# Kernel optimization log

Hardware: AMD Instinct MI355X
Metric: run time of the kernel (lower is better)

## Reference

```python
import jax, jax.numpy as jnp
import numpy as np

BATCH, FLAT_IN, PROJ_DIM, HEADS, ACT_DIM = 2048, 512, 256, 16384, 64


def setup_inputs() -> dict:
    key = jax.random.key(0)
    k1, k2, k3, k4 = jax.random.split(key, 4)
    state = jax.random.normal(k1, (BATCH, FLAT_IN), dtype=jnp.float32)
    random_projection = jax.random.normal(k2, (FLAT_IN, PROJ_DIM), dtype=jnp.float32)
    memories = jax.random.normal(k3, (HEADS, PROJ_DIM), dtype=jnp.float32)
    logits = jax.random.normal(k4, (HEADS, ACT_DIM), dtype=jnp.float32)
    return {"state": state, "random_projection": random_projection,
            "memories": memories, "logits": logits}


def reference(state, random_projection, memories, logits):
    # state: [B, flat_in] -> projected [B, proj_dim] (proj_dim branch of __call__)
    s = state.reshape(state.shape[0], -1) @ random_projection
    # sum(state[:,None] * memories[None,:], -1) == dot-product similarity GEMM
    similarities = jnp.einsum('bd,hd->bh', s, memories)  # [B, heads]
    closest = jnp.argmax(similarities, axis=1)           # [B]
    return logits[closest]                                # [B, act_dim]
```

## Files before the change

kernel.cpp:

```cpp
#include <hip/hip_runtime.h>

#define BATCH    2048
#define FLAT_IN  512
#define PROJ_DIM 256
#define HEADS    16384
#define ACT_DIM  64

typedef __attribute__((ext_vector_type(8))) short short8;
typedef _Float16 half8 __attribute__((ext_vector_type(8)));
typedef __attribute__((ext_vector_type(4))) float floatx4;

__device__ __forceinline__ unsigned short f2bf(float x) {
  unsigned u = __float_as_uint(x);
  u += 0x7fff + ((u >> 16) & 1);
  return (unsigned short)(u >> 16);
}
__device__ __forceinline__ float bf2f(unsigned short b) {
  return __uint_as_float(((unsigned)b) << 16);
}
__device__ __forceinline__ unsigned short f2h(float x) {
  _Float16 h = (_Float16)x;
  return __builtin_bit_cast(unsigned short, h);
}

__device__ __forceinline__ unsigned pack_key(float v, int h) {
  unsigned u = __float_as_uint(v);
  unsigned m = (unsigned)(((int)u) >> 31) | 0x80000000u;
  return ((u ^ m) & 0xFFFFC000u) | (unsigned)(16383 - h);
}

#define GLDS16(g, l)                                                          \
  __builtin_amdgcn_global_load_lds(                                           \
      (__attribute__((address_space(1))) void*)(void*)(g),                    \
      (__attribute__((address_space(3))) void*)(l), 16, 0, 0)

__global__ __launch_bounds__(256) void prep(
    const float* __restrict__ state, const float* __restrict__ rp,
    unsigned short* __restrict__ st_hi, unsigned short* __restrict__ st_mid,
    unsigned short* __restrict__ rpT_hi, unsigned short* __restrict__ rpT_mid)
{
  const int tid = threadIdx.x;
  const int b = blockIdx.x;
  if (b < 1024) {
    int i = b * 256 + tid;
    float4 v = ((const float4*)state)[i];
    ushort4 h, m;
    h.x = f2bf(v.x); m.x = f2bf(v.x - bf2f(h.x));
    h.y = f2bf(v.y); m.y = f2bf(v.y - bf2f(h.y));
    h.z = f2bf(v.z); m.z = f2bf(v.z - bf2f(h.z));
    h.w = f2bf(v.w); m.w = f2bf(v.w - bf2f(h.w));
    ((ushort4*)st_hi)[i]  = h;
    ((ushort4*)st_mid)[i] = m;
  } else {
    __shared__ float t[64][65];
    int bid = b - 1024;
    int k0 = (bid >> 2) * 64, n0 = (bid & 3) * 64;
#pragma unroll
    for (int it = 0; it < 16; ++it) {
      int lin = it * 256 + tid;
      int kr = lin >> 6, nc = lin & 63;
      t[kr][nc] = rp[(size_t)(k0 + kr) * PROJ_DIM + n0 + nc];
    }
    __syncthreads();
#pragma unroll
    for (int it = 0; it < 16; ++it) {
      int lin = it * 256 + tid;
      int nr = lin >> 6, kc = lin & 63;
      float v = t[kc][nr];
      unsigned short hh = f2bf(v);
      rpT_hi [(size_t)(n0 + nr) * FLAT_IN + k0 + kc] = hh;
      rpT_mid[(size_t)(n0 + nr) * FLAT_IN + k0 + kc] = f2bf(v - bf2f(hh));
    }
  }
}

__global__ __launch_bounds__(256, 2) void gemm_conv(
    const unsigned short* __restrict__ Ahi, const unsigned short* __restrict__ Amid,
    const unsigned short* __restrict__ Bhi, const unsigned short* __restrict__ Bmid,
    const float* __restrict__ mem,
    float* __restrict__ S, unsigned short* __restrict__ Sf16,
    unsigned short* __restrict__ mem_f16)
{
  const int tid = threadIdx.x;
  if (blockIdx.x >= 128) {
    int i2 = (blockIdx.x - 128) * 256 + tid;
    float4 x = ((const float4*)mem)[2 * i2];
    float4 y = ((const float4*)mem)[2 * i2 + 1];
    short8 o;
    o[0] = (short)f2h(x.x); o[1] = (short)f2h(x.y);
    o[2] = (short)f2h(x.z); o[3] = (short)f2h(x.w);
    o[4] = (short)f2h(y.x); o[5] = (short)f2h(y.y);
    o[6] = (short)f2h(y.z); o[7] = (short)f2h(y.w);
    ((short8*)mem_f16)[i2] = o;
    return;
  }

  __shared__ __align__(16) unsigned short sm[4][64 * 64];
  const int lane = tid & 63, w = tid >> 6;
  const int quad = lane >> 4, col = lane & 15;
  const int wm = (w >> 1) * 32, wn = (w & 1) * 32;
  const int g = blockIdx.x;
  const int m0 = (g & 31) * 64, n0 = (g >> 5) * 64;

  floatx4 acc[2][2];
#pragma unroll
  for (int i = 0; i < 2; ++i)
#pragma unroll
    for (int j = 0; j < 2; ++j) {
      acc[i][j][0] = 0.f; acc[i][j][1] = 0.f;
      acc[i][j][2] = 0.f; acc[i][j][3] = 0.f;
    }

  const int P0 = tid, P1 = tid + 256;
  const int r0 = P0 >> 3, kl0 = (P0 & 7) ^ (r0 & 7);
  const int r1 = P1 >> 3, kl1 = (P1 & 7) ^ (r1 & 7);

  for (int kc = 0; kc < FLAT_IN; kc += 64) {
    GLDS16(Ahi  + (size_t)(m0 + r0) * FLAT_IN + kc + kl0 * 8, &sm[0][P0 * 8]);
    GLDS16(Ahi  + (size_t)(m0 + r1) * FLAT_IN + kc + kl1 * 8, &sm[0][P1 * 8]);
    GLDS16(Amid + (size_t)(m0 + r0) * FLAT_IN + kc + kl0 * 8, &sm[1][P0 * 8]);
    GLDS16(Amid + (size_t)(m0 + r1) * FLAT_IN + kc + kl1 * 8, &sm[1][P1 * 8]);
    GLDS16(Bhi  + (size_t)(n0 + r0) * FLAT_IN + kc + kl0 * 8, &sm[2][P0 * 8]);
    GLDS16(Bhi  + (size_t)(n0 + r1) * FLAT_IN + kc + kl1 * 8, &sm[2][P1 * 8]);
    GLDS16(Bmid + (size_t)(n0 + r0) * FLAT_IN + kc + kl0 * 8, &sm[3][P0 * 8]);
    GLDS16(Bmid + (size_t)(n0 + r1) * FLAT_IN + kc + kl1 * 8, &sm[3][P1 * 8]);
    __syncthreads();

#pragma unroll
    for (int ks = 0; ks < 2; ++ks) {
      short8 bf[2][2];
#pragma unroll
      for (int j = 0; j < 2; ++j) {
        int rr = wn + j * 16 + col;
        int off = rr * 64 + (((ks * 4 + quad) ^ (rr & 7)) * 8);
        bf[j][0] = *(const short8*)&sm[2][off];
        bf[j][1] = *(const short8*)&sm[3][off];
      }
#pragma unroll
      for (int i = 0; i < 2; ++i) {
        int rr = wm + i * 16 + col;
        int off = rr * 64 + (((ks * 4 + quad) ^ (rr & 7)) * 8);
        short8 a0 = *(const short8*)&sm[0][off];
        short8 a1 = *(const short8*)&sm[1][off];
#pragma unroll
        for (int j = 0; j < 2; ++j) {
          acc[i][j] = __builtin_amdgcn_mfma_f32_16x16x32_bf16(a0, bf[j][0], acc[i][j], 0, 0, 0);
          acc[i][j] = __builtin_amdgcn_mfma_f32_16x16x32_bf16(a0, bf[j][1], acc[i][j], 0, 0, 0);
          acc[i][j] = __builtin_amdgcn_mfma_f32_16x16x32_bf16(a1, bf[j][0], acc[i][j], 0, 0, 0);
        }
      }
    }
    __syncthreads();
  }

#pragma unroll
  for (int i = 0; i < 2; ++i)
#pragma unroll
    for (int j = 0; j < 2; ++j)
#pragma unroll
      for (int r = 0; r < 4; ++r) {
        int row = m0 + wm + i * 16 + quad * 4 + r;
        int c   = n0 + wn + j * 16 + col;
        float v = acc[i][j][r];
        S   [(size_t)row * PROJ_DIM + c] = v;
        Sf16[(size_t)row * PROJ_DIM + c] = f2h(v);
      }
}

__global__ __launch_bounds__(512, 2) void sim_topk(
    const unsigned short* __restrict__ Af16,
    const unsigned short* __restrict__ Bf16,
    unsigned* __restrict__ part1)
{
  __shared__ __align__(16) unsigned short smA[256 * 64];
  __shared__ __align__(16) unsigned short smB[256 * 64];
  const int tid = threadIdx.x;
  const int lane = tid & 63, w = tid >> 6;
  const int quad = lane >> 4, col = lane & 15;
  const int wm = (w >> 2) * 128, wn = (w & 3) * 64;
  const int hc = blockIdx.x;
  const int h0 = hc * 256;
  const int m0 = blockIdx.y * 256;

  floatx4 acc[8][4];
#pragma unroll
  for (int i = 0; i < 8; ++i)
#pragma unroll
    for (int j = 0; j < 4; ++j) {
      acc[i][j][0] = 0.f; acc[i][j][1] = 0.f;
      acc[i][j][2] = 0.f; acc[i][j][3] = 0.f;
    }

  int rs[4], kl[4];
#pragma unroll
  for (int t = 0; t < 4; ++t) {
    int P = t * 512 + tid;
    rs[t] = P >> 3; kl[t] = (P & 7) ^ (rs[t] & 7);
  }

  for (int kc = 0; kc < PROJ_DIM; kc += 64) {
#pragma unroll
    for (int t = 0; t < 4; ++t)
      GLDS16(Af16 + (size_t)(m0 + rs[t]) * PROJ_DIM + kc + kl[t] * 8,
             &smA[(t * 512 + tid) * 8]);
#pragma unroll
    for (int t = 0; t < 4; ++t)
      GLDS16(Bf16 + (size_t)(h0 + rs[t]) * PROJ_DIM + kc + kl[t] * 8,
             &smB[(t * 512 + tid) * 8]);
    __syncthreads();

#pragma unroll
    for (int ks = 0; ks < 2; ++ks) {
      half8 a[8], bfr[4];
#pragma unroll
      for (int j = 0; j < 4; ++j) {
        int rr = wn + j * 16 + col;
        int off = rr * 64 + (((ks * 4 + quad) ^ (rr & 7)) * 8);
        bfr[j] = *(const half8*)&smB[off];
      }
#pragma unroll
      for (int i = 0; i < 8; ++i) {
        int rr = wm + i * 16 + col;
        int off = rr * 64 + (((ks * 4 + quad) ^ (rr & 7)) * 8);
        a[i] = *(const half8*)&smA[off];
      }
#pragma unroll
      for (int i = 0; i < 8; ++i)
#pragma unroll
        for (int j = 0; j < 4; ++j)
          acc[i][j] = __builtin_amdgcn_mfma_f32_16x16x32_f16(a[i], bfr[j], acc[i][j], 0, 0, 0);
    }
    __syncthreads();
  }

#pragma unroll
  for (int i = 0; i < 8; ++i)
#pragma unroll
    for (int r = 0; r < 4; ++r) {
      unsigned best = pack_key(acc[i][0][r], h0 + wn + col);
#pragma unroll
      for (int j = 1; j < 4; ++j) {
        unsigned k = pack_key(acc[i][j][r], h0 + wn + j * 16 + col);
        best = best > k ? best : k;
      }
#pragma unroll
      for (int m = 1; m <= 8; m <<= 1) {
        unsigned o = (unsigned)__shfl_xor((int)best, m);
        best = best > o ? best : o;
      }
      if (col == 0) {
        int row = m0 + wm + i * 16 + quad * 4 + r;
        part1[((size_t)row * 64 + hc) * 4 + (w & 3)] = best;
      }
    }
}

__global__ __launch_bounds__(64) void finalize(
    const unsigned* __restrict__ part1, const float* __restrict__ S,
    const float* __restrict__ Mem, const float* __restrict__ logits,
    float* __restrict__ out)
{
  const int row  = blockIdx.x;
  const int lane = threadIdx.x;

  unsigned k[4];
#pragma unroll
  for (int t = 0; t < 4; ++t)
    k[t] = part1[(size_t)row * 256 + t * 64 + lane];

  int cand[4]; float4 mv[4];
#pragma unroll
  for (int t = 0; t < 4; ++t) {
    unsigned lv = k[0];
#pragma unroll
    for (int q = 1; q < 4; ++q) lv = lv > k[q] ? lv : k[q];
#pragma unroll
    for (int d = 32; d; d >>= 1) {
      unsigned o = (unsigned)__shfl_xor((int)lv, d);
      lv = lv > o ? lv : o;
    }
    cand[t] = 16383 - (int)(lv & 16383u);
    mv[t] = ((const float4*)(Mem + (size_t)cand[t] * PROJ_DIM))[lane];
#pragma unroll
    for (int q = 0; q < 4; ++q)
      if (k[q] == lv) k[q] = 0;
  }

  float4 sv = ((const float4*)(S + (size_t)row * PROJ_DIM))[lane];
  float bestv = -3.4e38f; int besth = 0x7fffffff;
#pragma unroll
  for (int t = 0; t < 4; ++t) {
    float d = sv.x * mv[t].x + sv.y * mv[t].y + sv.z * mv[t].z + sv.w * mv[t].w;
#pragma unroll
    for (int s = 32; s; s >>= 1) d += __shfl_xor(d, s);
    if (d > bestv || (d == bestv && cand[t] < besth)) { bestv = d; besth = cand[t]; }
  }
  out[(size_t)row * ACT_DIM + lane] = logits[(size_t)besth * ACT_DIM + lane];
}

extern "C" void kernel_launch(void* const* d_in, const int* in_sizes, int n_in,
                              void* d_out, int out_size, void* d_ws, size_t ws_size,
                              hipStream_t stream) {
  const float* state  = (const float*)d_in[0];
  const float* rp     = (const float*)d_in[1];
  const float* mem    = (const float*)d_in[2];
  const float* logits = (const float*)d_in[3];
  float* out = (float*)d_out;

  char* ws = (char*)d_ws;
  unsigned short* st_hi   = (unsigned short*)(ws);
  unsigned short* st_mid  = (unsigned short*)(ws + (2u  << 20));
  unsigned short* rpT_hi  = (unsigned short*)(ws + (4u  << 20));
  unsigned short* rpT_mid = (unsigned short*)(ws + (4u  << 20) + (256u << 10));
  unsigned short* mem_f16 = (unsigned short*)(ws + (8u  << 20));
  float*          s       = (float*)(ws + (16u << 20));
  unsigned short* s_f16   = (unsigned short*)(ws + (18u << 20));
  unsigned*       part1   = (unsigned*)(ws + (20u << 20));

  prep<<<1056, 256, 0, stream>>>(state, rp, st_hi, st_mid, rpT_hi, rpT_mid);

  gemm_conv<<<2176, 256, 0, stream>>>(st_hi, st_mid, rpT_hi, rpT_mid, mem,
                                      s, s_f16, mem_f16);

  sim_topk<<<dim3(64, 8), 512, 0, stream>>>(s_f16, mem_f16, part1);

  finalize<<<BATCH, 64, 0, stream>>>(part1, s, mem, logits, out);
}
```

Before: 116.4 us.

## Double-buffer LDS tiles in similarity GEMM to overlap loads with MFMA

```diff
diff --git a/kernel.cpp b/kernel.cpp
--- a/kernel.cpp
+++ b/kernel.cpp
@@ -172,8 +172,8 @@
     const unsigned short* __restrict__ Bf16,
     unsigned* __restrict__ part1)
 {
-  __shared__ __align__(16) unsigned short smA[256 * 64];
-  __shared__ __align__(16) unsigned short smB[256 * 64];
+  __shared__ __align__(16) unsigned short smA[2][256 * 64];
+  __shared__ __align__(16) unsigned short smB[2][256 * 64];
   const int tid = threadIdx.x;
   const int lane = tid & 63, w = tid >> 6;
   const int quad = lane >> 4, col = lane & 15;
@@ -198,17 +198,28 @@
     rs[t] = P >> 3; kl[t] = (P & 7) ^ (rs[t] & 7);
   }
 
-  for (int kc = 0; kc < PROJ_DIM; kc += 64) {
-#pragma unroll
-    for (int t = 0; t < 4; ++t)
-      GLDS16(Af16 + (size_t)(m0 + rs[t]) * PROJ_DIM + kc + kl[t] * 8,
-             &smA[(t * 512 + tid) * 8]);
-#pragma unroll
-    for (int t = 0; t < 4; ++t)
-      GLDS16(Bf16 + (size_t)(h0 + rs[t]) * PROJ_DIM + kc + kl[t] * 8,
-             &smB[(t * 512 + tid) * 8]);
-    __syncthreads();
-
+#define STAGE_KT(kt)                                                          \
+  do {                                                                        \
+    const int _kc = (kt) * 64;                                                \
+    _Pragma("unroll")                                                         \
+    for (int t = 0; t < 4; ++t)                                               \
+      GLDS16(Af16 + (size_t)(m0 + rs[t]) * PROJ_DIM + _kc + kl[t] * 8,        \
+             &smA[(kt) & 1][(t * 512 + tid) * 8]);                            \
+    _Pragma("unroll")                                                         \
+    for (int t = 0; t < 4; ++t)                                               \
+      GLDS16(Bf16 + (size_t)(h0 + rs[t]) * PROJ_DIM + _kc + kl[t] * 8,        \
+             &smB[(kt) & 1][(t * 512 + tid) * 8]);                            \
+  } while (0)
+
+  STAGE_KT(0);
+  __syncthreads();
+
+#pragma unroll
+  for (int kt = 0; kt < 4; ++kt) {
+    if (kt < 3) STAGE_KT(kt + 1);
+
+    const unsigned short* A = smA[kt & 1];
+    const unsigned short* B = smB[kt & 1];
 #pragma unroll
     for (int ks = 0; ks < 2; ++ks) {
       half8 a[8], bfr[4];
@@ -216,13 +227,13 @@
       for (int j = 0; j < 4; ++j) {
         int rr = wn + j * 16 + col;
         int off = rr * 64 + (((ks * 4 + quad) ^ (rr & 7)) * 8);
-        bfr[j] = *(const half8*)&smB[off];
+        bfr[j] = *(const half8*)&B[off];
       }
 #pragma unroll
       for (int i = 0; i < 8; ++i) {
         int rr = wm + i * 16 + col;
         int off = rr * 64 + (((ks * 4 + quad) ^ (rr & 7)) * 8);
-        a[i] = *(const half8*)&smA[off];
+        a[i] = *(const half8*)&A[off];
       }
 #pragma unroll
       for (int i = 0; i < 8; ++i)
@@ -230,8 +241,10 @@
         for (int j = 0; j < 4; ++j)
           acc[i][j] = __builtin_amdgcn_mfma_f32_16x16x32_f16(a[i], bfr[j], acc[i][j], 0, 0, 0);
     }
-    __syncthreads();
-  }
+
+    if (kt < 3) __syncthreads();
+  }
+#undef STAGE_KT
 
 #pragma unroll
   for (int i = 0; i < 8; ++i)
```

After: 116.5 us, median of 2. About the same (+0.0%).
